# Kernel tuning notes

Measured on AMD Instinct MI355X. Metric: run time of the kernel, lower is better.

Reference implementation:

```python
import jax, jax.numpy as jnp
import numpy as np

NUM_EMBEDDINGS = 1024
EMBEDDING_DIM = 256
COMMITMENT_COST = 0.25


def setup_inputs() -> dict:
    key = jax.random.key(0)
    k_z, k_e = jax.random.split(key)
    z = jax.random.normal(k_z, (16, EMBEDDING_DIM, 4096), dtype=jnp.float32)
    # nn.Embedding init: uniform(-1/K, 1/K)
    emb = jax.random.uniform(
        k_e, (NUM_EMBEDDINGS, EMBEDDING_DIM), dtype=jnp.float32,
        minval=-1.0 / NUM_EMBEDDINGS, maxval=1.0 / NUM_EMBEDDINGS)
    return {"z": z, "emb": emb}


def reference(z, emb):
    # z: [B, D, T] -> [B, T, D]
    zt = jnp.transpose(z, (0, 2, 1))
    B, T, D = zt.shape
    flat = zt.reshape(-1, D)  # [N, D]
    dists = (jnp.sum(flat * flat, axis=1, keepdims=True)
             + jnp.sum(emb * emb, axis=1)
             - 2.0 * jnp.matmul(flat, emb.T))
    idx = jnp.argmin(dists, axis=1)          # [N]
    quantized = emb[idx].reshape(B, T, D)    # gather + reshape
    e_latent_loss = jnp.mean((jax.lax.stop_gradient(quantized) - zt) ** 2)
    q_latent_loss = jnp.mean((quantized - jax.lax.stop_gradient(zt)) ** 2)
    loss = q_latent_loss + COMMITMENT_COST * e_latent_loss
    # straight-through estimator
    quantized_st = zt + jax.lax.stop_gradient(quantized - zt)
    return jnp.transpose(quantized_st, (0, 2, 1)), loss
```

## Files before the change

### kernel.cpp

```cpp
#include <hip/hip_runtime.h>
#include <stdint.h>

#define B_   16
#define D_   256
#define T_   4096
#define K_   1024
#define N_   (B_ * T_)
#define BM   64

typedef __attribute__((ext_vector_type(4))) float floatx4;
typedef __attribute__((ext_vector_type(2))) float floatx2;
typedef __attribute__((ext_vector_type(2))) long longx2;

__global__ __launch_bounds__(256) void emb_prep(const float* __restrict__ emb,
                                                uint32_t* __restrict__ embf8,
                                                float* __restrict__ esqh,
                                                float* __restrict__ lossp) {
    int w = threadIdx.x >> 6, lane = threadIdx.x & 63;
    int k = blockIdx.x * 4 + w;
    float4 v = ((const float4*)emb)[k * 64 + lane];
    float a0 = v.x * 1024.f, a1 = v.y * 1024.f, a2 = v.z * 1024.f, a3 = v.w * 1024.f;
    int p = __builtin_amdgcn_cvt_pk_fp8_f32(a0, a1, 0, false);
    p = __builtin_amdgcn_cvt_pk_fp8_f32(a2, a3, p, true);
    int kk = lane >> 3, quad = (lane >> 1) & 3;
    int widx = (k >> 4) * 1024 + (kk >> 1) * 256 + (quad * 16 + (k & 15)) * 4
             + (kk & 1) * 2 + (lane & 1);
    embf8[widx] = (uint32_t)p;
    float ss = a0 * a0 + a1 * a1 + a2 * a2 + a3 * a3;
    #pragma unroll
    for (int off = 32; off; off >>= 1) ss += __shfl_xor(ss, off, 64);
    if (lane == 0) esqh[k] = ss * (0.5f / 1024.f);
    if (blockIdx.x == 0 && threadIdx.x == 0) *lossp = 0.f;
}

__global__ __launch_bounds__(256, 3) void vq_main(const float* __restrict__ z,
                                                  const uint32_t* __restrict__ embf8,
                                                  const float* __restrict__ esqh,
                                                  float* __restrict__ out0,
                                                  float* __restrict__ lossp) {
    __shared__ __align__(16) unsigned char xs[BM * 256];
    __shared__ float wvals[4][BM];
    __shared__ int   pidx[BM];
    __shared__ float zred[4];

    int tid  = threadIdx.x;
    int lane = tid & 63, w = tid >> 6;
    int ml   = lane & 15, quad = lane >> 4;
    int blk  = blockIdx.x;
    int b    = blk >> 6;
    int t0   = (blk & 63) * BM;
    const float* zb = z + (size_t)b * (D_ * T_) + t0;

    float zsq = 0.f;
    {
        int t = lane, hf = (t >> 4) & 1;
        #pragma unroll 2
        for (int j = 0; j < 8; ++j) {
            int dgrp = w + 4 * j;
            int d0 = dgrp * 8;
            float f0 = zb[(d0 + 0) * T_ + t];
            float f1 = zb[(d0 + 1) * T_ + t];
            float f2 = zb[(d0 + 2) * T_ + t];
            float f3 = zb[(d0 + 3) * T_ + t];
            float f4 = zb[(d0 + 4) * T_ + t];
            float f5 = zb[(d0 + 5) * T_ + t];
            float f6 = zb[(d0 + 6) * T_ + t];
            float f7 = zb[(d0 + 7) * T_ + t];
            zsq += f0*f0 + f1*f1 + f2*f2 + f3*f3 + f4*f4 + f5*f5 + f6*f6 + f7*f7;
            uint32_t p0 = (uint32_t)__builtin_amdgcn_cvt_pk_fp8_f32(f0, f1, 0, false);
            p0 = (uint32_t)__builtin_amdgcn_cvt_pk_fp8_f32(f2, f3, (int)p0, true);
            uint32_t p1 = (uint32_t)__builtin_amdgcn_cvt_pk_fp8_f32(f4, f5, 0, false);
            p1 = (uint32_t)__builtin_amdgcn_cvt_pk_fp8_f32(f6, f7, (int)p1, true);
            int c = dgrp >> 1, h = dgrp & 1;
            *(uint2*)&xs[t * 256 + ((c ^ (t & 15)) << 4) + ((h ^ hf) << 3)] =
                make_uint2(p0, p1);
        }
    }
    __syncthreads();

    long afr[4][8];
    #pragma unroll
    for (int s = 0; s < 4; ++s) {
        int pnt = s * 16 + ml;
        #pragma unroll
        for (int kk = 0; kk < 8; ++kk) {
            int c = 2 * kk + (quad >> 1), h = quad & 1;
            afr[s][kk] = *(const long*)&xs[pnt * 256 + ((c ^ ml) << 4) + ((h ^ (s & 1)) << 3)];
        }
    }

    float bv[4][4];
    #pragma unroll
    for (int s = 0; s < 4; ++s)
        #pragma unroll
        for (int i = 0; i < 4; ++i) bv[s][i] = 1e30f;

    int ct0 = w * 16;
    const char* ebL = (const char*)embf8 + (size_t)ct0 * 4096 + (size_t)lane * 16;
    const unsigned hi_mask = 0xFFFFFC00u;
    #pragma unroll 2
    for (int j = 0; j < 16; ++j) {
        const char* p = ebL + (size_t)j * 4096;
        longx2 qq[4];
        #pragma unroll
        for (int i = 0; i < 4; ++i)
            qq[i] = *(const longx2*)(p + i * 1024);
        float eh = esqh[(ct0 + j) * 16 + ml];
        floatx4 a0 = {0,0,0,0}, a1 = {0,0,0,0}, a2 = {0,0,0,0}, a3 = {0,0,0,0};
        #pragma unroll
        for (int i = 0; i < 4; ++i) {
            long bf0 = qq[i][0], bf1 = qq[i][1];
            a0 = __builtin_amdgcn_mfma_f32_16x16x32_fp8_fp8(afr[0][2*i],     bf0, a0, 0, 0, 0);
            a1 = __builtin_amdgcn_mfma_f32_16x16x32_fp8_fp8(afr[1][2*i],     bf0, a1, 0, 0, 0);
            a2 = __builtin_amdgcn_mfma_f32_16x16x32_fp8_fp8(afr[2][2*i],     bf0, a2, 0, 0, 0);
            a3 = __builtin_amdgcn_mfma_f32_16x16x32_fp8_fp8(afr[3][2*i],     bf0, a3, 0, 0, 0);
            a0 = __builtin_amdgcn_mfma_f32_16x16x32_fp8_fp8(afr[0][2*i + 1], bf1, a0, 0, 0, 0);
            a1 = __builtin_amdgcn_mfma_f32_16x16x32_fp8_fp8(afr[1][2*i + 1], bf1, a1, 0, 0, 0);
            a2 = __builtin_amdgcn_mfma_f32_16x16x32_fp8_fp8(afr[2][2*i + 1], bf1, a2, 0, 0, 0);
            a3 = __builtin_amdgcn_mfma_f32_16x16x32_fp8_fp8(afr[3][2*i + 1], bf1, a3, 0, 0, 0);
        }
        unsigned cbits = (unsigned)((ct0 + j) * 16 + ml);
        #pragma unroll
        for (int i = 0; i < 4; ++i) {
            float d0 = eh - a0[i];
            bv[0][i] = fminf(bv[0][i], __uint_as_float((__float_as_uint(d0) & hi_mask) | cbits));
            float d1 = eh - a1[i];
            bv[1][i] = fminf(bv[1][i], __uint_as_float((__float_as_uint(d1) & hi_mask) | cbits));
            float d2 = eh - a2[i];
            bv[2][i] = fminf(bv[2][i], __uint_as_float((__float_as_uint(d2) & hi_mask) | cbits));
            float d3 = eh - a3[i];
            bv[3][i] = fminf(bv[3][i], __uint_as_float((__float_as_uint(d3) & hi_mask) | cbits));
        }
    }

    #pragma unroll
    for (int s = 0; s < 4; ++s)
        #pragma unroll
        for (int i = 0; i < 4; ++i) {
            float v = bv[s][i];
            #pragma unroll
            for (int off = 1; off < 16; off <<= 1)
                v = fminf(v, __shfl_xor(v, off, 64));
            if (ml == 0) wvals[w][s * 16 + quad * 4 + i] = v;
        }
    #pragma unroll
    for (int off = 32; off; off >>= 1) zsq += __shfl_xor(zsq, off, 64);
    if (lane == 0) zred[w] = zsq;
    __syncthreads();

    if (tid < 64) {
        int t = tid;
        float wv = fminf(fminf(wvals[0][t], wvals[1][t]),
                         fminf(wvals[2][t], wvals[3][t]));
        pidx[t] = (int)(__float_as_uint(wv) & 1023u);
        float lsum = wv;
        #pragma unroll
        for (int off = 32; off; off >>= 1) lsum += __shfl_xor(lsum, off, 64);
        if (t == 0) {
            float tot = zred[0] + zred[1] + zred[2] + zred[3] + lsum * (2.0f / 1024.f);
            atomicAdd(lossp, tot * (1.25f / 16777216.0f));
        }
    }
    __syncthreads();

    #pragma unroll
    for (int m = 0; m < 4; ++m) {
        int t = (tid >> 4) + 16 * m;
        int g = tid & 15;
        int code = pidx[t];
        const char* src = (const char*)embf8 + (size_t)(code >> 4) * 4096
                        + (g >> 2) * 1024 + ((g & 3) * 16 + (code & 15)) * 16;
        uint4 v = *(const uint4*)src;
        *(uint4*)&xs[t * 256 + ((g ^ (t & 15)) << 4)] = v;
    }
    __syncthreads();

    float* ob = out0 + (size_t)b * (D_ * T_) + t0;
    {
        int t = lane;
        #pragma unroll
        for (int jj = 0; jj < 4; ++jj) {
            int g = w + 4 * jj;
            uint4 v = *(const uint4*)&xs[t * 256 + ((g ^ (t & 15)) << 4)];
            uint32_t wd[4] = {v.x, v.y, v.z, v.w};
            #pragma unroll
            for (int u = 0; u < 4; ++u) {
                int kk = (g >> 2) * 2 + (u >> 1);
                int d0 = kk * 32 + (g & 3) * 8 + (u & 1) * 4;
                floatx2 lo = __builtin_amdgcn_cvt_pk_f32_fp8((int)wd[u], false);
                floatx2 hi = __builtin_amdgcn_cvt_pk_f32_fp8((int)wd[u], true);
                ob[(d0 + 0) * T_ + t] = lo[0] * (1.f / 1024.f);
                ob[(d0 + 1) * T_ + t] = lo[1] * (1.f / 1024.f);
                ob[(d0 + 2) * T_ + t] = hi[0] * (1.f / 1024.f);
                ob[(d0 + 3) * T_ + t] = hi[1] * (1.f / 1024.f);
            }
        }
    }
}

extern "C" void kernel_launch(void* const* d_in, const int* in_sizes, int n_in,
                              void* d_out, int out_size, void* d_ws, size_t ws_size,
                              hipStream_t stream) {
    (void)in_sizes; (void)n_in; (void)out_size; (void)ws_size;
    const float* z   = (const float*)d_in[0];
    const float* emb = (const float*)d_in[1];

    uint32_t* embf8 = (uint32_t*)d_ws;
    float*    esqh  = (float*)((char*)d_ws + (size_t)K_ * D_);

    float* out0  = (float*)d_out;
    float* lossp = out0 + (size_t)N_ * D_;

    emb_prep<<<K_ / 4, 256, 0, stream>>>(emb, embf8, esqh, lossp);
    vq_main<<<N_ / BM, 256, 0, stream>>>(z, embf8, esqh, out0, lossp);
}
```

Measured before the change: 143.6 us.

## Use scaled 16x16x128 FP8 MFMA with 256-row tiles and codebook split

Result: slower. 164.2 us (+14.3%).

```diff
diff --git a/kernel.cpp b/kernel.cpp
--- a/kernel.cpp
+++ b/kernel.cpp
@@ -6,11 +6,13 @@
 #define T_   4096
 #define K_   1024
 #define N_   (B_ * T_)
-#define BM   64
+#define BM   256
 
 typedef __attribute__((ext_vector_type(4))) float floatx4;
 typedef __attribute__((ext_vector_type(2))) float floatx2;
-typedef __attribute__((ext_vector_type(2))) long longx2;
+typedef __attribute__((ext_vector_type(8))) int  intx8;
+
+#define SCALE1 0x7F7F7F7F
 
 __global__ __launch_bounds__(256) void emb_prep(const float* __restrict__ emb,
                                                 uint32_t* __restrict__ embf8,
@@ -19,12 +21,13 @@
     int w = threadIdx.x >> 6, lane = threadIdx.x & 63;
     int k = blockIdx.x * 4 + w;
     float4 v = ((const float4*)emb)[k * 64 + lane];
-    float a0 = v.x * 1024.f, a1 = v.y * 1024.f, a2 = v.z * 1024.f, a3 = v.w * 1024.f;
+    float a0 = v.x * -1024.f, a1 = v.y * -1024.f, a2 = v.z * -1024.f, a3 = v.w * -1024.f;
     int p = __builtin_amdgcn_cvt_pk_fp8_f32(a0, a1, 0, false);
     p = __builtin_amdgcn_cvt_pk_fp8_f32(a2, a3, p, true);
-    int kk = lane >> 3, quad = (lane >> 1) & 3;
-    int widx = (k >> 4) * 1024 + (kk >> 1) * 256 + (quad * 16 + (k & 15)) * 4
-             + (kk & 1) * 2 + (lane & 1);
+    int d0 = lane * 4;
+    int hh = d0 >> 7, pc = (d0 >> 4) & 1, quad = (d0 >> 5) & 3;
+    int widx = (k >> 4) * 1024 + hh * 512 + pc * 256
+             + (quad * 16 + (k & 15)) * 4 + ((d0 & 15) >> 2);
     embf8[widx] = (uint32_t)p;
     float ss = a0 * a0 + a1 * a1 + a2 * a2 + a3 * a3;
     #pragma unroll
@@ -33,31 +36,32 @@
     if (blockIdx.x == 0 && threadIdx.x == 0) *lossp = 0.f;
 }
 
-__global__ __launch_bounds__(256, 3) void vq_main(const float* __restrict__ z,
+__global__ __launch_bounds__(768, 3) void vq_main(const float* __restrict__ z,
                                                   const uint32_t* __restrict__ embf8,
                                                   const float* __restrict__ esqh,
                                                   float* __restrict__ out0,
                                                   float* __restrict__ lossp) {
     __shared__ __align__(16) unsigned char xs[BM * 256];
-    __shared__ float wvals[4][BM];
+    __shared__ float wvals[3][BM];
     __shared__ int   pidx[BM];
-    __shared__ float zred[4];
+    __shared__ float zred[12];
+    __shared__ float lred[4];
 
     int tid  = threadIdx.x;
     int lane = tid & 63, w = tid >> 6;
     int ml   = lane & 15, quad = lane >> 4;
+    int sg   = w & 3, cp = w >> 2;
     int blk  = blockIdx.x;
-    int b    = blk >> 6;
-    int t0   = (blk & 63) * BM;
+    int b    = blk >> 4;
+    int t0   = (blk & 15) * BM;
     const float* zb = z + (size_t)b * (D_ * T_) + t0;
 
     float zsq = 0.f;
-    {
-        int t = lane, hf = (t >> 4) & 1;
-        #pragma unroll 2
-        for (int j = 0; j < 8; ++j) {
-            int dgrp = w + 4 * j;
-            int d0 = dgrp * 8;
+    #pragma unroll
+    for (int it = 0; it < 11; ++it) {
+        int u = tid + it * 768;
+        if (u < 8192) {
+            int t = u >> 5, dgrp = u & 31, d0 = dgrp * 8;
             float f0 = zb[(d0 + 0) * T_ + t];
             float f1 = zb[(d0 + 1) * T_ + t];
             float f2 = zb[(d0 + 2) * T_ + t];
@@ -72,20 +76,26 @@
             uint32_t p1 = (uint32_t)__builtin_amdgcn_cvt_pk_fp8_f32(f4, f5, 0, false);
             p1 = (uint32_t)__builtin_amdgcn_cvt_pk_fp8_f32(f6, f7, (int)p1, true);
             int c = dgrp >> 1, h = dgrp & 1;
-            *(uint2*)&xs[t * 256 + ((c ^ (t & 15)) << 4) + ((h ^ hf) << 3)] =
+            *(uint2*)&xs[t * 256 + ((c ^ (t & 15)) << 4) + ((h ^ ((t >> 4) & 1)) << 3)] =
                 make_uint2(p0, p1);
         }
     }
     __syncthreads();
 
-    long afr[4][8];
+    intx8 afr[4][2];
     #pragma unroll
     for (int s = 0; s < 4; ++s) {
-        int pnt = s * 16 + ml;
-        #pragma unroll
-        for (int kk = 0; kk < 8; ++kk) {
-            int c = 2 * kk + (quad >> 1), h = quad & 1;
-            afr[s][kk] = *(const long*)&xs[pnt * 256 + ((c ^ ml) << 4) + ((h ^ (s & 1)) << 3)];
+        int pnt = (sg * 4 + s) * 16 + ml;
+        #pragma unroll
+        for (int hh = 0; hh < 2; ++hh) {
+            union { long l[4]; intx8 v; } af;
+            #pragma unroll
+            for (int rr = 0; rr < 4; ++rr) {
+                int c = hh * 8 + quad * 2 + (rr >> 1);
+                af.l[rr] = *(const long*)&xs[pnt * 256 + ((c ^ ml) << 4)
+                                             + (((rr & 1) ^ (s & 1)) << 3)];
+            }
+            afr[s][hh] = af.v;
         }
     }
 
@@ -95,41 +105,35 @@
         #pragma unroll
         for (int i = 0; i < 4; ++i) bv[s][i] = 1e30f;
 
-    int ct0 = w * 16;
-    const char* ebL = (const char*)embf8 + (size_t)ct0 * 4096 + (size_t)lane * 16;
+    int jstart = (cp == 0) ? 0 : (cp == 1 ? 22 : 43);
+    int jend   = (cp == 0) ? 22 : (cp == 1 ? 43 : 64);
+    const char* ebL = (const char*)embf8 + (size_t)lane * 16;
     const unsigned hi_mask = 0xFFFFFC00u;
     #pragma unroll 2
-    for (int j = 0; j < 16; ++j) {
-        const char* p = ebL + (size_t)j * 4096;
-        longx2 qq[4];
-        #pragma unroll
-        for (int i = 0; i < 4; ++i)
-            qq[i] = *(const longx2*)(p + i * 1024);
-        float eh = esqh[(ct0 + j) * 16 + ml];
-        floatx4 a0 = {0,0,0,0}, a1 = {0,0,0,0}, a2 = {0,0,0,0}, a3 = {0,0,0,0};
+    for (int j = jstart; j < jend; ++j) {
+        const char* pB = ebL + (size_t)j * 4096;
+        union { uint4 u[2]; intx8 v; } b0, b1;
+        b0.u[0] = *(const uint4*)(pB);
+        b0.u[1] = *(const uint4*)(pB + 1024);
+        b1.u[0] = *(const uint4*)(pB + 2048);
+        b1.u[1] = *(const uint4*)(pB + 3072);
+        float eh = esqh[j * 16 + ml];
+        unsigned cbits = (unsigned)(j * 16 + ml);
+        floatx4 a0 = {eh, eh, eh, eh}, a1 = a0, a2 = a0, a3 = a0;
+        a0 = __builtin_amdgcn_mfma_scale_f32_16x16x128_f8f6f4(afr[0][0], b0.v, a0, 0, 0, 0, SCALE1, 0, SCALE1);
+        a1 = __builtin_amdgcn_mfma_scale_f32_16x16x128_f8f6f4(afr[1][0], b0.v, a1, 0, 0, 0, SCALE1, 0, SCALE1);
+        a2 = __builtin_amdgcn_mfma_scale_f32_16x16x128_f8f6f4(afr[2][0], b0.v, a2, 0, 0, 0, SCALE1, 0, SCALE1);
+        a3 = __builtin_amdgcn_mfma_scale_f32_16x16x128_f8f6f4(afr[3][0], b0.v, a3, 0, 0, 0, SCALE1, 0, SCALE1);
+        a0 = __builtin_amdgcn_mfma_scale_f32_16x16x128_f8f6f4(afr[0][1], b1.v, a0, 0, 0, 0, SCALE1, 0, SCALE1);
+        a1 = __builtin_amdgcn_mfma_scale_f32_16x16x128_f8f6f4(afr[1][1], b1.v, a1, 0, 0, 0, SCALE1, 0, SCALE1);
+        a2 = __builtin_amdgcn_mfma_scale_f32_16x16x128_f8f6f4(afr[2][1], b1.v, a2, 0, 0, 0, SCALE1, 0, SCALE1);
+        a3 = __builtin_amdgcn_mfma_scale_f32_16x16x128_f8f6f4(afr[3][1], b1.v, a3, 0, 0, 0, SCALE1, 0, SCALE1);
         #pragma unroll
         for (int i = 0; i < 4; ++i) {
-            long bf0 = qq[i][0], bf1 = qq[i][1];
-            a0 = __builtin_amdgcn_mfma_f32_16x16x32_fp8_fp8(afr[0][2*i],     bf0, a0, 0, 0, 0);
-            a1 = __builtin_amdgcn_mfma_f32_16x16x32_fp8_fp8(afr[1][2*i],     bf0, a1, 0, 0, 0);
-            a2 = __builtin_amdgcn_mfma_f32_16x16x32_fp8_fp8(afr[2][2*i],     bf0, a2, 0, 0, 0);
-            a3 = __builtin_amdgcn_mfma_f32_16x16x32_fp8_fp8(afr[3][2*i],     bf0, a3, 0, 0, 0);
-            a0 = __builtin_amdgcn_mfma_f32_16x16x32_fp8_fp8(afr[0][2*i + 1], bf1, a0, 0, 0, 0);
-            a1 = __builtin_amdgcn_mfma_f32_16x16x32_fp8_fp8(afr[1][2*i + 1], bf1, a1, 0, 0, 0);
-            a2 = __builtin_amdgcn_mfma_f32_16x16x32_fp8_fp8(afr[2][2*i + 1], bf1, a2, 0, 0, 0);
-            a3 = __builtin_amdgcn_mfma_f32_16x16x32_fp8_fp8(afr[3][2*i + 1], bf1, a3, 0, 0, 0);
-        }
-        unsigned cbits = (unsigned)((ct0 + j) * 16 + ml);
-        #pragma unroll
-        for (int i = 0; i < 4; ++i) {
-            float d0 = eh - a0[i];
-            bv[0][i] = fminf(bv[0][i], __uint_as_float((__float_as_uint(d0) & hi_mask) | cbits));
-            float d1 = eh - a1[i];
-            bv[1][i] = fminf(bv[1][i], __uint_as_float((__float_as_uint(d1) & hi_mask) | cbits));
-            float d2 = eh - a2[i];
-            bv[2][i] = fminf(bv[2][i], __uint_as_float((__float_as_uint(d2) & hi_mask) | cbits));
-            float d3 = eh - a3[i];
-            bv[3][i] = fminf(bv[3][i], __uint_as_float((__float_as_uint(d3) & hi_mask) | cbits));
+            bv[0][i] = fminf(bv[0][i], __uint_as_float((__float_as_uint(a0[i]) & hi_mask) | cbits));
+            bv[1][i] = fminf(bv[1][i], __uint_as_float((__float_as_uint(a1[i]) & hi_mask) | cbits));
+            bv[2][i] = fminf(bv[2][i], __uint_as_float((__float_as_uint(a2[i]) & hi_mask) | cbits));
+            bv[3][i] = fminf(bv[3][i], __uint_as_float((__float_as_uint(a3[i]) & hi_mask) | cbits));
         }
     }
 
@@ -141,58 +145,65 @@
             #pragma unroll
             for (int off = 1; off < 16; off <<= 1)
                 v = fminf(v, __shfl_xor(v, off, 64));
-            if (ml == 0) wvals[w][s * 16 + quad * 4 + i] = v;
+            if (ml == 0) wvals[cp][(sg * 4 + s) * 16 + quad * 4 + i] = v;
         }
     #pragma unroll
     for (int off = 32; off; off >>= 1) zsq += __shfl_xor(zsq, off, 64);
     if (lane == 0) zred[w] = zsq;
     __syncthreads();
 
-    if (tid < 64) {
+    if (tid < BM) {
         int t = tid;
-        float wv = fminf(fminf(wvals[0][t], wvals[1][t]),
-                         fminf(wvals[2][t], wvals[3][t]));
+        float wv = fminf(fminf(wvals[0][t], wvals[1][t]), wvals[2][t]);
         pidx[t] = (int)(__float_as_uint(wv) & 1023u);
         float lsum = wv;
         #pragma unroll
         for (int off = 32; off; off >>= 1) lsum += __shfl_xor(lsum, off, 64);
-        if (t == 0) {
-            float tot = zred[0] + zred[1] + zred[2] + zred[3] + lsum * (2.0f / 1024.f);
-            atomicAdd(lossp, tot * (1.25f / 16777216.0f));
-        }
-    }
-    __syncthreads();
-
-    #pragma unroll
-    for (int m = 0; m < 4; ++m) {
-        int t = (tid >> 4) + 16 * m;
-        int g = tid & 15;
-        int code = pidx[t];
-        const char* src = (const char*)embf8 + (size_t)(code >> 4) * 4096
-                        + (g >> 2) * 1024 + ((g & 3) * 16 + (code & 15)) * 16;
-        uint4 v = *(const uint4*)src;
-        *(uint4*)&xs[t * 256 + ((g ^ (t & 15)) << 4)] = v;
+        if (lane == 0) lred[w] = lsum;
+    }
+    __syncthreads();
+    if (tid == 0) {
+        float zs = 0.f;
+        #pragma unroll
+        for (int i = 0; i < 12; ++i) zs += zred[i];
+        float ls = lred[0] + lred[1] + lred[2] + lred[3];
+        atomicAdd(lossp, (zs + ls * (2.0f / 1024.f)) * (1.25f / 16777216.0f));
+    }
+
+    #pragma unroll
+    for (int it = 0; it < 6; ++it) {
+        int u = tid + it * 768;
+        if (u < 4096) {
+            int t = u >> 4, g = u & 15;
+            int hh = g >> 3, pc = (g >> 2) & 1, qd = g & 3;
+            int code = pidx[t];
+            const char* src = (const char*)embf8 + (size_t)(code >> 4) * 4096
+                            + hh * 2048 + pc * 1024 + (qd * 16 + (code & 15)) * 16;
+            uint4 v = *(const uint4*)src;
+            *(uint4*)&xs[t * 256 + ((g ^ (t & 15)) << 4)] = v;
+        }
     }
     __syncthreads();
 
     float* ob = out0 + (size_t)b * (D_ * T_) + t0;
-    {
-        int t = lane;
-        #pragma unroll
-        for (int jj = 0; jj < 4; ++jj) {
-            int g = w + 4 * jj;
+    #pragma unroll
+    for (int it = 0; it < 6; ++it) {
+        int u = tid + it * 768;
+        if (u < 4096) {
+            int t = u & 255, g = u >> 8;
             uint4 v = *(const uint4*)&xs[t * 256 + ((g ^ (t & 15)) << 4)];
             uint32_t wd[4] = {v.x, v.y, v.z, v.w};
+            int hh = g >> 3, pc = (g >> 2) & 1, qd = g & 3;
+            int db = hh * 128 + qd * 32 + pc * 16;
             #pragma unroll
-            for (int u = 0; u < 4; ++u) {
-                int kk = (g >> 2) * 2 + (u >> 1);
-                int d0 = kk * 32 + (g & 3) * 8 + (u & 1) * 4;
-                floatx2 lo = __builtin_amdgcn_cvt_pk_f32_fp8((int)wd[u], false);
-                floatx2 hi = __builtin_amdgcn_cvt_pk_f32_fp8((int)wd[u], true);
-                ob[(d0 + 0) * T_ + t] = lo[0] * (1.f / 1024.f);
-                ob[(d0 + 1) * T_ + t] = lo[1] * (1.f / 1024.f);
-                ob[(d0 + 2) * T_ + t] = hi[0] * (1.f / 1024.f);
-                ob[(d0 + 3) * T_ + t] = hi[1] * (1.f / 1024.f);
+            for (int u4 = 0; u4 < 4; ++u4) {
+                int d0 = db + u4 * 4;
+                floatx2 lo = __builtin_amdgcn_cvt_pk_f32_fp8((int)wd[u4], false);
+                floatx2 hi = __builtin_amdgcn_cvt_pk_f32_fp8((int)wd[u4], true);
+                ob[(d0 + 0) * T_ + t] = lo[0] * (-1.f / 1024.f);
+                ob[(d0 + 1) * T_ + t] = lo[1] * (-1.f / 1024.f);
+                ob[(d0 + 2) * T_ + t] = hi[0] * (-1.f / 1024.f);
+                ob[(d0 + 3) * T_ + t] = hi[1] * (-1.f / 1024.f);
             }
         }
     }
@@ -212,5 +223,5 @@
     float* lossp = out0 + (size_t)N_ * D_;
 
     emb_prep<<<K_ / 4, 256, 0, stream>>>(emb, embf8, esqh, lossp);
-    vq_main<<<N_ / BM, 256, 0, stream>>>(z, embf8, esqh, out0, lossp);
+    vq_main<<<N_ / BM, 768, 0, stream>>>(z, embf8, esqh, out0, lossp);
 }
```
